# Kernel tuning notes

Hardware: AMD Instinct MI355X
Metric: run time of the kernel (lower is better)

The kernel has to match this reference:

```python
import jax, jax.numpy as jnp
import numpy as np

NUM_HEADS = 6
KERNEL = 5
EPS = 1e-6


def _neighbor_idx(L, k):
    # NATTEN neighborhood: window start clamped so every query has exactly k neighbors
    starts = jnp.clip(jnp.arange(L) - k // 2, 0, L - k)
    return starts[:, None] + jnp.arange(k)  # [L, k]


def ada_rmsnorm(x, scale, w1, b1, w2, b2):
    # x: [B,C,D,H,W]; RMS over spatial dims, gamma from channel means via small MLP
    rms = jnp.sqrt(jnp.mean(x * x, axis=(2, 3, 4), keepdims=True) + EPS)
    xn = x / rms
    stats = jnp.mean(x, axis=(2, 3, 4))                 # [B,C]
    h = jax.nn.relu(stats @ w1.T + b1)                  # [B,2C]
    gamma = jax.nn.sigmoid(h @ w2.T + b2)               # [B,C]
    return xn * (scale * gamma[:, :, None, None, None])


def reference(x, scale1, n1_w1, n1_b1, n1_w2, n1_b2,
              qkv_w, qkv_b, proj_w, proj_b,
              scale2, n2_w1, n2_b1, n2_w2, n2_b2,
              mlp_w1, mlp_b1, mlp_w2, mlp_b2):
    B, C, D, H, W = x.shape
    nh_, k_ = NUM_HEADS, KERNEL
    hd = C // nh_
    K3 = k_ ** 3

    # --- norm1 + neighborhood attention ---
    h = ada_rmsnorm(x, scale1, n1_w1, n1_b1, n1_w2, n1_b2)
    t = jnp.transpose(h, (0, 2, 3, 4, 1))               # [B,D,H,W,C]
    qkv = t @ qkv_w.T + qkv_b                           # [B,D,H,W,3C]
    q, k, v = jnp.split(qkv, 3, axis=-1)
    q = q.reshape(B, D, H, W, nh_, hd)
    k = k.reshape(B, D, H, W, nh_, hd)
    v = v.reshape(B, D, H, W, nh_, hd)

    iD = _neighbor_idx(D, k_)
    iH = _neighbor_idx(H, k_)
    iW = _neighbor_idx(W, k_)
    nd = iD[:, None, None, :, None, None]               # [D,1,1,k,1,1]
    nhh = iH[None, :, None, None, :, None]              # [1,H,1,1,k,1]
    nw = iW[None, None, :, None, None, :]               # [1,1,W,1,1,k]

    k_nb = k[:, nd, nhh, nw].reshape(B, D, H, W, K3, nh_, hd)
    v_nb = v[:, nd, nhh, nw].reshape(B, D, H, W, K3, nh_, hd)

    scale_qk = hd ** -0.5
    scores = jnp.einsum('bdhwnc,bdhwknc->bdhwnk', q, k_nb) * scale_qk  # [B,D,H,W,heads,K3]
    p = jax.nn.softmax(scores, axis=-1)
    o = jnp.einsum('bdhwnk,bdhwknc->bdhwnc', p, v_nb).reshape(B, D, H, W, C)
    o = o @ proj_w.T + proj_b                            # output projection
    x = x + jnp.transpose(o, (0, 4, 1, 2, 3))

    # --- norm2 + 1x1-conv MLP (GELU exact) ---
    h2 = ada_rmsnorm(x, scale2, n2_w1, n2_b1, n2_w2, n2_b2)
    m = jnp.einsum('oc,bcdhw->bodhw', mlp_w1, h2) + mlp_b1[None, :, None, None, None]
    m = jax.nn.gelu(m, approximate=False)
    m = jnp.einsum('oc,bcdhw->bodhw', mlp_w2, m) + mlp_b2[None, :, None, None, None]
    return x + m


def setup_inputs() -> dict:
    key = jax.random.key(0)
    ks = jax.random.split(key, 16)
    B, C, D, H, W = 1, 192, 16, 16, 16
    hid = 2 * C
    mlp_h = int(4.0 * C)
    s = 0.02
    inp = {
        'x': jax.random.normal(ks[0], (B, C, D, H, W), jnp.float32),
        'scale1': jnp.ones((1, C, 1, 1, 1), jnp.float32),
        'n1_w1': jax.random.normal(ks[1], (hid, C), jnp.float32) * s,
        'n1_b1': jnp.zeros((hid,), jnp.float32),
        'n1_w2': jax.random.normal(ks[2], (C, hid), jnp.float32) * s,
        'n1_b2': jnp.zeros((C,), jnp.float32),
        'qkv_w': jax.random.normal(ks[3], (3 * C, C), jnp.float32) * s,
        'qkv_b': jnp.zeros((3 * C,), jnp.float32),
        'proj_w': jax.random.normal(ks[4], (C, C), jnp.float32) * s,
        'proj_b': jnp.zeros((C,), jnp.float32),
        'scale2': jnp.ones((1, C, 1, 1, 1), jnp.float32),
        'n2_w1': jax.random.normal(ks[5], (hid, C), jnp.float32) * s,
        'n2_b1': jnp.zeros((hid,), jnp.float32),
        'n2_w2': jax.random.normal(ks[6], (C, hid), jnp.float32) * s,
        'n2_b2': jnp.zeros((C,), jnp.float32),
        'mlp_w1': jax.random.normal(ks[7], (mlp_h, C), jnp.float32) * s,
        'mlp_b1': jnp.zeros((mlp_h,), jnp.float32),
        'mlp_w2': jax.random.normal(ks[8], (C, mlp_h), jnp.float32) * s,
        'mlp_b2': jnp.zeros((C,), jnp.float32),
    }
    return inp
```

## Files before the change

### kernel.cpp

```cpp
#include <hip/hip_runtime.h>
#include <hip/hip_bf16.h>
#include <cmath>


#define NPOS 4096
#define C_CH 192
#define NB   512

typedef __bf16 bf16x8 __attribute__((ext_vector_type(8)));
typedef __bf16 bf16x4 __attribute__((ext_vector_type(4)));
typedef float  f32x4  __attribute__((ext_vector_type(4)));

__device__ __forceinline__ float bflo(unsigned int u) {
    union { unsigned int i; float f; } c; c.i = u << 16; return c.f;
}
__device__ __forceinline__ float bfhi(unsigned int u) {
    union { unsigned int i; float f; } c; c.i = u & 0xffff0000u; return c.f;
}


__device__ __forceinline__ void pre_sync(unsigned* bar, int grp) {
    __syncthreads();
    if (threadIdx.x == 0) {
        unsigned* arr    = bar + 128 + grp * 16;
        unsigned* master = bar + 256;
        unsigned* go     = bar + 272 + grp * 16;
        unsigned prev = __hip_atomic_fetch_add(arr, 1u, __ATOMIC_RELAXED,
                                               __HIP_MEMORY_SCOPE_AGENT);
        if (prev == 63u) {
            __hip_atomic_fetch_add(master, 1u, __ATOMIC_RELAXED,
                                   __HIP_MEMORY_SCOPE_AGENT);
            while (__hip_atomic_load(master, __ATOMIC_RELAXED,
                                     __HIP_MEMORY_SCOPE_AGENT) < 8u)
                __builtin_amdgcn_s_sleep(2);
            __hip_atomic_store(go, 1u, __ATOMIC_RELAXED, __HIP_MEMORY_SCOPE_AGENT);
        }
        while (__hip_atomic_load(go, __ATOMIC_RELAXED,
                                 __HIP_MEMORY_SCOPE_AGENT) == 0u)
            __builtin_amdgcn_s_sleep(2);
    }
    __syncthreads();
}

__device__ __forceinline__ void grid_sync(unsigned* bar, int idx, int xcc,
                                          unsigned myPop, unsigned nx) {
    __syncthreads();
    if (threadIdx.x == 0) {
        unsigned* base   = bar + 512 + idx * 512;
        unsigned* arr    = base + xcc * 16;
        unsigned* master = base + 128;
        unsigned* go     = base + 144 + xcc * 16;
        unsigned prev = __hip_atomic_fetch_add(arr, 1u, __ATOMIC_RELAXED,
                                               __HIP_MEMORY_SCOPE_AGENT);
        if (prev == myPop - 1u) {
            __hip_atomic_fetch_add(master, 1u, __ATOMIC_RELEASE,
                                   __HIP_MEMORY_SCOPE_AGENT);
            while (__hip_atomic_load(master, __ATOMIC_RELAXED,
                                     __HIP_MEMORY_SCOPE_AGENT) < nx)
                __builtin_amdgcn_s_sleep(2);
            __hip_atomic_store(go, 1u, __ATOMIC_RELAXED, __HIP_MEMORY_SCOPE_AGENT);
        }
        while (__hip_atomic_load(go, __ATOMIC_RELAXED,
                                 __HIP_MEMORY_SCOPE_AGENT) == 0u)
            __builtin_amdgcn_s_sleep(2);
    }
    __syncthreads();
}

__device__ __forceinline__ void conv_unit(const float* __restrict__ src,
                                          __bf16* __restrict__ dst, int base)
{
    int i = (base * 256 + (int)threadIdx.x) * 4;
    float4 v = *(const float4*)(src + i);
    bf16x4 o = { (__bf16)v.x, (__bf16)v.y, (__bf16)v.z, (__bf16)v.w };
    *(bf16x4*)(dst + i) = o;
}

__device__ void stats_unit(float* sm, const float* __restrict__ x,
                           float* __restrict__ sums, float* __restrict__ sumsq, int c)
{
    const float4* xc = (const float4*)(x + (size_t)c * NPOS);
    float a = 0.f, a2 = 0.f;
    for (int i = threadIdx.x; i < NPOS / 4; i += 256) {
        float4 v = xc[i];
        a  += v.x + v.y + v.z + v.w;
        a2 += v.x * v.x + v.y * v.y + v.z * v.z + v.w * v.w;
    }
    #pragma unroll
    for (int off = 32; off > 0; off >>= 1) {
        a  += __shfl_down(a, off);
        a2 += __shfl_down(a2, off);
    }
    float* ls = sm; float* ls2 = sm + 4;
    int wid = threadIdx.x >> 6;
    if ((threadIdx.x & 63) == 0) { ls[wid] = a; ls2[wid] = a2; }
    __syncthreads();
    if (threadIdx.x == 0) {
        float t = 0.f, t2 = 0.f;
        #pragma unroll
        for (int w = 0; w < 4; w++) { t += ls[w]; t2 += ls2[w]; }
        sums[c] = t; sumsq[c] = t2;
    }
    __syncthreads();
}

__device__ void convx_body(float* sm, const float* __restrict__ x,
    const float* __restrict__ sums, const float* __restrict__ sumsq,
    const float* __restrict__ scale,
    const __bf16* __restrict__ w1b, const float* __restrict__ b1,
    const __bf16* __restrict__ w2b, const float* __restrict__ b2,
    __bf16* __restrict__ xb, int p0)
{
    float* stats = sm;
    float* h     = sm + 192;
    float* gsl   = sm + 576;
    float* lds   = sm + 768;
    int t = threadIdx.x;

    if (t < C_CH)
        stats[t] = __hip_atomic_load((const float*)&sums[t], __ATOMIC_RELAXED,
                                     __HIP_MEMORY_SCOPE_AGENT) * (1.0f / (float)NPOS);
    __syncthreads();
    for (int j = t; j < 384; j += 256) {
        float acc = b1[j];
        const __bf16* wr = w1b + (size_t)j * C_CH;
        #pragma unroll 4
        for (int c = 0; c < C_CH; c += 8) {
            bf16x8 w8 = *(const bf16x8*)(wr + c);
            acc += (float)w8[0] * stats[c]     + (float)w8[1] * stats[c + 1]
                 + (float)w8[2] * stats[c + 2] + (float)w8[3] * stats[c + 3]
                 + (float)w8[4] * stats[c + 4] + (float)w8[5] * stats[c + 5]
                 + (float)w8[6] * stats[c + 6] + (float)w8[7] * stats[c + 7];
        }
        h[j] = fmaxf(acc, 0.0f);
    }
    __syncthreads();
    if (t < C_CH) {
        float acc = b2[t];
        const __bf16* wr = w2b + (size_t)t * 384;
        #pragma unroll 4
        for (int j = 0; j < 384; j += 8) {
            bf16x8 w8 = *(const bf16x8*)(wr + j);
            acc += (float)w8[0] * h[j]     + (float)w8[1] * h[j + 1]
                 + (float)w8[2] * h[j + 2] + (float)w8[3] * h[j + 3]
                 + (float)w8[4] * h[j + 4] + (float)w8[5] * h[j + 5]
                 + (float)w8[6] * h[j + 6] + (float)w8[7] * h[j + 7];
        }
        float g = 1.0f / (1.0f + __expf(-acc));
        float sq = __hip_atomic_load((const float*)&sumsq[t], __ATOMIC_RELAXED,
                                     __HIP_MEMORY_SCOPE_AGENT);
        float rms = sqrtf(sq * (1.0f / (float)NPOS) + 1e-6f);
        gsl[t] = scale[t] * g / rms;
    }
    __syncthreads();
    for (int idx = t; idx < 192 * 4; idx += 256) {
        int row = idx >> 2, p4 = idx & 3;
        float4 v = *(const float4*)(x + (size_t)row * NPOS + p0 + p4 * 4);
        float g = gsl[row];
        lds[row * 17 + p4 * 4 + 0] = v.x * g;
        lds[row * 17 + p4 * 4 + 1] = v.y * g;
        lds[row * 17 + p4 * 4 + 2] = v.z * g;
        lds[row * 17 + p4 * 4 + 3] = v.w * g;
    }
    __syncthreads();
    for (int idx = t; idx < 48 * 16; idx += 256) {
        int c4 = idx >> 4, p = idx & 15;
        bf16x4 o;
        #pragma unroll
        for (int j = 0; j < 4; j++) o[j] = (__bf16)lds[(c4 * 4 + j) * 17 + p];
        *(bf16x4*)(xb + (size_t)(p0 + p) * 192 + c4 * 4) = o;
    }
    __syncthreads();
}

template <int K, int EPI>
__device__ void gemm_tile(__bf16* al, __bf16* bl, int bx, int by,
    const __bf16* __restrict__ W, const float* __restrict__ bias,
    const __bf16* __restrict__ X, void* __restrict__ out,
    const float* __restrict__ resid, int M, __bf16* __restrict__ out_kv,
    float* __restrict__ s2sum, float* __restrict__ s2sq)
{
    constexpr int KC  = 192;
    constexpr int LDA = 200;
    int t    = threadIdx.x;
    int lane = t & 63;
    int wv   = t >> 6;
    int r16  = lane & 15;
    int quad = lane >> 4;
    int wvm  = wv >> 1;
    int wvn  = wv & 1;
    int mBase = by * 64;
    int nBase = bx * 64;

    f32x4 acc[2][2];
    #pragma unroll
    for (int i = 0; i < 2; i++)
        #pragma unroll
        for (int j = 0; j < 2; j++)
            acc[i][j] = (f32x4){0.f, 0.f, 0.f, 0.f};

    for (int k0 = 0; k0 < K; k0 += KC) {
        #pragma unroll
        for (int it = 0; it < 6; it++) {
            int c = it * 256 + t;
            int row = c / 24, off = c - row * 24;
            bf16x8 va = *(const bf16x8*)(W + (size_t)(mBase + row) * K + k0 + off * 8);
            *(bf16x8*)(al + row * LDA + off * 8) = va;
            bf16x8 vb = *(const bf16x8*)(X + (size_t)(nBase + row) * K + k0 + off * 8);
            *(bf16x8*)(bl + row * LDA + off * 8) = vb;
        }
        __syncthreads();
        #pragma unroll
        for (int ks = 0; ks < KC / 32; ks++) {
            bf16x8 a0 = *(const bf16x8*)(al + (wvm * 32 + r16) * LDA + ks * 32 + quad * 8);
            bf16x8 a1 = *(const bf16x8*)(al + (wvm * 32 + 16 + r16) * LDA + ks * 32 + quad * 8);
            bf16x8 b0 = *(const bf16x8*)(bl + (wvn * 32 + r16) * LDA + ks * 32 + quad * 8);
            bf16x8 b1 = *(const bf16x8*)(bl + (wvn * 32 + 16 + r16) * LDA + ks * 32 + quad * 8);
            acc[0][0] = __builtin_amdgcn_mfma_f32_16x16x32_bf16(a0, b0, acc[0][0], 0, 0, 0);
            acc[0][1] = __builtin_amdgcn_mfma_f32_16x16x32_bf16(a0, b1, acc[0][1], 0, 0, 0);
            acc[1][0] = __builtin_amdgcn_mfma_f32_16x16x32_bf16(a1, b0, acc[1][0], 0, 0, 0);
            acc[1][1] = __builtin_amdgcn_mfma_f32_16x16x32_bf16(a1, b1, acc[1][1], 0, 0, 0);
        }
        __syncthreads();
    }

    #pragma unroll
    for (int rt = 0; rt < 2; rt++) {
        int m0 = mBase + wvm * 32 + rt * 16 + quad * 4;
        float b0 = bias[m0], b1v = bias[m0 + 1], b2v = bias[m0 + 2], b3v = bias[m0 + 3];
        float ss[4] = {0.f, 0.f, 0.f, 0.f}, sq[4] = {0.f, 0.f, 0.f, 0.f};
        #pragma unroll
        for (int ct = 0; ct < 2; ct++) {
            int n = nBase + wvn * 32 + ct * 16 + r16;
            f32x4 a4 = acc[rt][ct];
            float g0 = a4[0] + b0, g1 = a4[1] + b1v, g2 = a4[2] + b2v, g3 = a4[3] + b3v;
            if (EPI == 0) {
                int sect = m0 / 192;
                int o0 = m0 - sect * 192;
                if (sect == 0) {
                    const float qs = 0.17677669529663687f;
                    *(float4*)((float*)out + (size_t)n * 192 + o0) =
                        make_float4(g0 * qs, g1 * qs, g2 * qs, g3 * qs);
                } else {
                    bf16x4 kvv = { (__bf16)g0, (__bf16)g1, (__bf16)g2, (__bf16)g3 };
                    *(bf16x4*)(out_kv + (size_t)n * 384 + (o0 >> 2) * 8 + (sect - 1) * 4) = kvv;
                }
            } else if (EPI == 2 || EPI == 4) {
                float* o = (float*)out;
                size_t i0 = (size_t)m0 * NPOS + n;
                float v0 = g0 + resid[i0];
                float v1 = g1 + resid[i0 + NPOS];
                float v2 = g2 + resid[i0 + 2 * NPOS];
                float v3 = g3 + resid[i0 + 3 * NPOS];
                o[i0] = v0; o[i0 + NPOS] = v1; o[i0 + 2 * NPOS] = v2; o[i0 + 3 * NPOS] = v3;
                if (EPI == 4) {
                    ss[0] += v0; sq[0] += v0 * v0;
                    ss[1] += v1; sq[1] += v1 * v1;
                    ss[2] += v2; sq[2] += v2 * v2;
                    ss[3] += v3; sq[3] += v3 * v3;
                }
            } else {
                bf16x4 v;
                v[0] = (__bf16)(0.5f * g0 * (1.0f + erff(g0 * 0.7071067811865475f)));
                v[1] = (__bf16)(0.5f * g1 * (1.0f + erff(g1 * 0.7071067811865475f)));
                v[2] = (__bf16)(0.5f * g2 * (1.0f + erff(g2 * 0.7071067811865475f)));
                v[3] = (__bf16)(0.5f * g3 * (1.0f + erff(g3 * 0.7071067811865475f)));
                *(bf16x4*)((__bf16*)out + (size_t)n * M + m0) = v;
            }
        }
        if (EPI == 4) {
            #pragma unroll
            for (int j = 0; j < 4; j++) {
                float s = ss[j], s2v = sq[j];
                #pragma unroll
                for (int off = 8; off >= 1; off >>= 1) {
                    s   += __shfl_down(s, off);
                    s2v += __shfl_down(s2v, off);
                }
                if (r16 == 0) {
                    atomicAdd(&s2sum[m0 + j], s);
                    atomicAdd(&s2sq[m0 + j], s2v);
                }
            }
        }
    }
}

__device__ __forceinline__ void attn_unit(const float* __restrict__ q,
    const __bf16* __restrict__ kv, __bf16* __restrict__ o, int unit)
{
    int t = threadIdx.x;
    int pairIdx = unit * 8 + (t >> 5);
    int sg   = (t >> 3) & 3;
    int lane = t & 7;
    int pos = pairIdx / 6;
    int head = pairIdx - pos * 6;
    int wq = pos & 15;
    int hq = (pos >> 4) & 15;
    int dq = pos >> 8;
    int d0 = min(max(dq - 2, 0), 11);
    int h0 = min(max(hq - 2, 0), 11);
    int w0 = min(max(wq - 2, 0), 11);

    const __bf16* kvb = kv + head * 64 + lane * 8;
    float4 q4 = *(const float4*)(q + (size_t)pos * 192 + head * 32 + lane * 4);

    float l = 0.0f;
    float4 acc = make_float4(0.f, 0.f, 0.f, 0.f);

    for (int dh = sg; dh < 25; dh += 4) {
        int di = dh / 5;
        int hi = dh - di * 5;
        int np0 = (d0 + di) * 256 + (h0 + hi) * 16 + w0;
        const __bf16* p = kvb + (size_t)np0 * 384;
        #pragma unroll
        for (int wi = 0; wi < 5; wi++) {
            uint4 u = *(const uint4*)p;
            float s = q4.x * bflo(u.x) + q4.y * bfhi(u.x)
                    + q4.z * bflo(u.y) + q4.w * bfhi(u.y);
            s += __shfl_xor(s, 1);
            s += __shfl_xor(s, 2);
            s += __shfl_xor(s, 4);
            float pr = __expf(s);
            l += pr;
            acc.x += pr * bflo(u.z);
            acc.y += pr * bfhi(u.z);
            acc.z += pr * bflo(u.w);
            acc.w += pr * bfhi(u.w);
            p += 384;
        }
    }

    #pragma unroll
    for (int off = 8; off <= 16; off <<= 1) {
        l     += __shfl_xor(l, off);
        acc.x += __shfl_xor(acc.x, off);
        acc.y += __shfl_xor(acc.y, off);
        acc.z += __shfl_xor(acc.z, off);
        acc.w += __shfl_xor(acc.w, off);
    }

    if (sg == 0) {
        float rl = 1.0f / l;
        bf16x4 ov = { (__bf16)(acc.x * rl), (__bf16)(acc.y * rl),
                      (__bf16)(acc.z * rl), (__bf16)(acc.w * rl) };
        *(bf16x4*)(o + (size_t)pos * 192 + head * 32 + lane * 4) = ov;
    }
}

__global__ __launch_bounds__(256) void fused(
    const float* __restrict__ x, const float* __restrict__ scale1,
    const float* __restrict__ n1_w1, const float* __restrict__ n1_b1,
    const float* __restrict__ n1_w2, const float* __restrict__ n1_b2,
    const float* __restrict__ qkv_w, const float* __restrict__ qkv_b,
    const float* __restrict__ proj_w, const float* __restrict__ proj_b,
    const float* __restrict__ scale2,
    const float* __restrict__ n2_w1, const float* __restrict__ n2_b1,
    const float* __restrict__ n2_w2, const float* __restrict__ n2_b2,
    const float* __restrict__ mlp_w1, const float* __restrict__ mlp_b1,
    const float* __restrict__ mlp_w2, const float* __restrict__ mlp_b2,
    float* __restrict__ ws, float* __restrict__ x2)
{
    __shared__ __align__(16) char smraw[51200];
    __bf16* al  = (__bf16*)smraw;
    __bf16* bl  = al + 64 * 200;
    float*  smf = (float*)smraw;

    float*  q_buf   = ws;
    __bf16* kv_buf  = (__bf16*)(ws + 786432);
    __bf16* xb      = (__bf16*)(ws + 2359296);
    __bf16* o_attn  = (__bf16*)(ws + 2752512);
    __bf16* qkv_wb  = (__bf16*)(ws + 3145728);
    __bf16* proj_wb = qkv_wb + 110592;
    __bf16* m1_wb   = proj_wb + 36864;
    __bf16* m2_wb   = m1_wb + 147456;
    float*  sums1   = ws + 3366912;
    float*  sumsq1  = ws + 3367104;
    float*  sums2   = ws + 3367296;
    float*  sumsq2  = ws + 3367488;
    __bf16* n1w1b   = (__bf16*)(ws + 3367680);
    __bf16* n1w2b   = n1w1b + 73728;
    __bf16* n2w1b   = n1w2b + 73728;
    __bf16* n2w2b   = n2w1b + 73728;
    unsigned* bar   = (unsigned*)(ws + 3515136);
    __bf16* m_buf   = (__bf16*)(ws + 3520512);
    __bf16* xb2     = (__bf16*)(ws + 5093376);

    int bid = blockIdx.x;
    int t   = threadIdx.x;

    int xcc = __builtin_amdgcn_s_getreg(63508) & 7;

    if (t == 0)
        __hip_atomic_fetch_add(bar + xcc * 16, 1u, __ATOMIC_RELAXED,
                               __HIP_MEMORY_SCOPE_AGENT);
    pre_sync(bar, bid & 7);
    unsigned myPop = 0, nx = 0;
    if (t == 0) {
        myPop = __hip_atomic_load(bar + xcc * 16, __ATOMIC_RELAXED,
                                  __HIP_MEMORY_SCOPE_AGENT);
        #pragma unroll
        for (int xi = 0; xi < 8; xi++)
            nx += (__hip_atomic_load(bar + xi * 16, __ATOMIC_RELAXED,
                                     __HIP_MEMORY_SCOPE_AGENT) > 0u) ? 1u : 0u;
    }

    for (int u = bid; u < 913; u += NB) {
        if      (u < 108) conv_unit(qkv_w,  qkv_wb, u);
        else if (u < 144) conv_unit(proj_w, proj_wb, u - 108);
        else if (u < 288) conv_unit(mlp_w1, m1_wb, u - 144);
        else if (u < 432) conv_unit(mlp_w2, m2_wb, u - 288);
        else if (u < 504) conv_unit(n1_w1,  n1w1b, u - 432);
        else if (u < 576) conv_unit(n1_w2,  n1w2b, u - 504);
        else if (u < 648) conv_unit(n2_w1,  n2w1b, u - 576);
        else if (u < 720) conv_unit(n2_w2,  n2w2b, u - 648);
        else if (u < 912) stats_unit(smf, x, sums1, sumsq1, u - 720);
        else {
            if (t < 192) {
                __hip_atomic_store(&sums2[t], 0.f, __ATOMIC_RELAXED,
                                   __HIP_MEMORY_SCOPE_AGENT);
                __hip_atomic_store(&sumsq2[t], 0.f, __ATOMIC_RELAXED,
                                   __HIP_MEMORY_SCOPE_AGENT);
            }
        }
    }
    grid_sync(bar, 0, xcc, myPop, nx);

    if (bid < 256)
        convx_body(smf, x, sums1, sumsq1, scale1, n1w1b, n1_b1, n1w2b, n1_b2, xb, bid * 16);
    grid_sync(bar, 1, xcc, myPop, nx);

    for (int tile = bid; tile < 576; tile += NB)
        gemm_tile<192, 0>(al, bl, tile & 63, tile >> 6, qkv_wb, qkv_b, xb,
                          (void*)q_buf, nullptr, 576, kv_buf, nullptr, nullptr);
    grid_sync(bar, 2, xcc, myPop, nx);

    {
        int base = (bid & 7) * 384 + (bid >> 3) * 6;
        for (int i = 0; i < 6; i++)
            attn_unit(q_buf, kv_buf, o_attn, base + i);
    }
    grid_sync(bar, 3, xcc, myPop, nx);

    if (bid < 192)
        gemm_tile<192, 4>(al, bl, bid & 63, bid >> 6, proj_wb, proj_b, o_attn,
                          (void*)x2, x, 192, nullptr, sums2, sumsq2);
    grid_sync(bar, 4, xcc, myPop, nx);

    if (bid < 256)
        convx_body(smf, x2, sums2, sumsq2, scale2, n2w1b, n2_b1, n2w2b, n2_b2, xb2, bid * 16);
    grid_sync(bar, 5, xcc, myPop, nx);

    for (int tile = bid; tile < 768; tile += NB)
        gemm_tile<192, 3>(al, bl, tile & 63, tile >> 6, m1_wb, mlp_b1, xb2,
                          (void*)m_buf, nullptr, 768, nullptr, nullptr, nullptr);
    grid_sync(bar, 6, xcc, myPop, nx);

    if (bid < 192)
        gemm_tile<768, 2>(al, bl, bid & 63, bid >> 6, m2_wb, mlp_b2, m_buf,
                          (void*)x2, x2, 192, nullptr, nullptr, nullptr);
}

extern "C" void kernel_launch(void* const* d_in, const int* in_sizes, int n_in,
                              void* d_out, int out_size, void* d_ws, size_t ws_size,
                              hipStream_t stream)
{
    const float* x      = (const float*)d_in[0];
    const float* scale1 = (const float*)d_in[1];
    const float* n1_w1  = (const float*)d_in[2];
    const float* n1_b1  = (const float*)d_in[3];
    const float* n1_w2  = (const float*)d_in[4];
    const float* n1_b2  = (const float*)d_in[5];
    const float* qkv_w  = (const float*)d_in[6];
    const float* qkv_b  = (const float*)d_in[7];
    const float* proj_w = (const float*)d_in[8];
    const float* proj_b = (const float*)d_in[9];
    const float* scale2 = (const float*)d_in[10];
    const float* n2_w1  = (const float*)d_in[11];
    const float* n2_b1  = (const float*)d_in[12];
    const float* n2_w2  = (const float*)d_in[13];
    const float* n2_b2  = (const float*)d_in[14];
    const float* mlp_w1 = (const float*)d_in[15];
    const float* mlp_b1 = (const float*)d_in[16];
    const float* mlp_w2 = (const float*)d_in[17];
    const float* mlp_b2 = (const float*)d_in[18];

    float* ws = (float*)d_ws;
    float* x2 = (float*)d_out;

    hipMemsetAsync(ws + 3515136, 0, 4096 * sizeof(unsigned), stream);

    fused<<<NB, 256, 0, stream>>>(x, scale1, n1_w1, n1_b1, n1_w2, n1_b2,
                                  qkv_w, qkv_b, proj_w, proj_b,
                                  scale2, n2_w1, n2_b1, n2_w2, n2_b2,
                                  mlp_w1, mlp_b1, mlp_w2, mlp_b2,
                                  ws, x2);
}
```

Measured before the change: 202.0 us.

## Fold adaptive RMSNorm scale into GEMM weights and drop two grid syncs

The per-channel RMSNorm gain is now applied to the weight tile as it is loaded into the qkv and MLP1 GEMMs. This lets the raw input transpose to bf16 run in the preprocessing phase, and the projection GEMM epilogue writes the bf16 transposed residual output directly. That removes the two standalone convx phases and two grid-wide barriers. In exchange every block recomputes the small gain MLP redundantly, and rounding changes slightly because scaling happens after bf16 conversion of x and on bf16 weights.

Measured after the change: 205.7 us. Within noise of the previous version (+1.8%).

```diff
diff --git a/kernel.cpp b/kernel.cpp
--- a/kernel.cpp
+++ b/kernel.cpp
@@ -104,19 +104,39 @@
     __syncthreads();
 }
 
-__device__ void convx_body(float* sm, const float* __restrict__ x,
+__device__ void transpose_unit(float* sm, const float* __restrict__ x,
+                               __bf16* __restrict__ xb, int p0)
+{
+    float* lds = sm;
+    int t = threadIdx.x;
+    for (int idx = t; idx < 192 * 4; idx += 256) {
+        int row = idx >> 2, p4 = idx & 3;
+        float4 v = *(const float4*)(x + (size_t)row * NPOS + p0 + p4 * 4);
+        lds[row * 17 + p4 * 4 + 0] = v.x;
+        lds[row * 17 + p4 * 4 + 1] = v.y;
+        lds[row * 17 + p4 * 4 + 2] = v.z;
+        lds[row * 17 + p4 * 4 + 3] = v.w;
+    }
+    __syncthreads();
+    for (int idx = t; idx < 48 * 16; idx += 256) {
+        int c4 = idx >> 4, p = idx & 15;
+        bf16x4 o;
+        #pragma unroll
+        for (int j = 0; j < 4; j++) o[j] = (__bf16)lds[(c4 * 4 + j) * 17 + p];
+        *(bf16x4*)(xb + (size_t)(p0 + p) * 192 + c4 * 4) = o;
+    }
+    __syncthreads();
+}
+
+__device__ void compute_gsl(float* scratch, float* gslOut,
     const float* __restrict__ sums, const float* __restrict__ sumsq,
     const float* __restrict__ scale,
     const __bf16* __restrict__ w1b, const float* __restrict__ b1,
-    const __bf16* __restrict__ w2b, const float* __restrict__ b2,
-    __bf16* __restrict__ xb, int p0)
-{
-    float* stats = sm;
-    float* h     = sm + 192;
-    float* gsl   = sm + 576;
-    float* lds   = sm + 768;
+    const __bf16* __restrict__ w2b, const float* __restrict__ b2)
+{
+    float* stats = scratch;
+    float* h     = scratch + 192;
     int t = threadIdx.x;
-
     if (t < C_CH)
         stats[t] = __hip_atomic_load((const float*)&sums[t], __ATOMIC_RELAXED,
                                      __HIP_MEMORY_SCOPE_AGENT) * (1.0f / (float)NPOS);
@@ -150,35 +170,19 @@
         float sq = __hip_atomic_load((const float*)&sumsq[t], __ATOMIC_RELAXED,
                                      __HIP_MEMORY_SCOPE_AGENT);
         float rms = sqrtf(sq * (1.0f / (float)NPOS) + 1e-6f);
-        gsl[t] = scale[t] * g / rms;
-    }
-    __syncthreads();
-    for (int idx = t; idx < 192 * 4; idx += 256) {
-        int row = idx >> 2, p4 = idx & 3;
-        float4 v = *(const float4*)(x + (size_t)row * NPOS + p0 + p4 * 4);
-        float g = gsl[row];
-        lds[row * 17 + p4 * 4 + 0] = v.x * g;
-        lds[row * 17 + p4 * 4 + 1] = v.y * g;
-        lds[row * 17 + p4 * 4 + 2] = v.z * g;
-        lds[row * 17 + p4 * 4 + 3] = v.w * g;
-    }
-    __syncthreads();
-    for (int idx = t; idx < 48 * 16; idx += 256) {
-        int c4 = idx >> 4, p = idx & 15;
-        bf16x4 o;
-        #pragma unroll
-        for (int j = 0; j < 4; j++) o[j] = (__bf16)lds[(c4 * 4 + j) * 17 + p];
-        *(bf16x4*)(xb + (size_t)(p0 + p) * 192 + c4 * 4) = o;
-    }
-    __syncthreads();
-}
-
-template <int K, int EPI>
-__device__ void gemm_tile(__bf16* al, __bf16* bl, int bx, int by,
+        gslOut[t] = scale[t] * g / rms;
+    }
+    __syncthreads();
+}
+
+template <int K, int EPI, bool SCALEA>
+__device__ void gemm_tile(__bf16* al, __bf16* bl, const float* gslLds,
+    int bx, int by,
     const __bf16* __restrict__ W, const float* __restrict__ bias,
     const __bf16* __restrict__ X, void* __restrict__ out,
     const float* __restrict__ resid, int M, __bf16* __restrict__ out_kv,
-    float* __restrict__ s2sum, float* __restrict__ s2sq)
+    float* __restrict__ s2sum, float* __restrict__ s2sq,
+    __bf16* __restrict__ xb2o)
 {
     constexpr int KC  = 192;
     constexpr int LDA = 200;
@@ -205,6 +209,11 @@
             int c = it * 256 + t;
             int row = c / 24, off = c - row * 24;
             bf16x8 va = *(const bf16x8*)(W + (size_t)(mBase + row) * K + k0 + off * 8);
+            if (SCALEA) {
+                #pragma unroll
+                for (int j = 0; j < 8; j++)
+                    va[j] = (__bf16)((float)va[j] * gslLds[off * 8 + j]);
+            }
             *(bf16x8*)(al + row * LDA + off * 8) = va;
             bf16x8 vb = *(const bf16x8*)(X + (size_t)(nBase + row) * K + k0 + off * 8);
             *(bf16x8*)(bl + row * LDA + off * 8) = vb;
@@ -254,6 +263,8 @@
                 float v3 = g3 + resid[i0 + 3 * NPOS];
                 o[i0] = v0; o[i0 + NPOS] = v1; o[i0 + 2 * NPOS] = v2; o[i0 + 3 * NPOS] = v3;
                 if (EPI == 4) {
+                    bf16x4 xv = { (__bf16)v0, (__bf16)v1, (__bf16)v2, (__bf16)v3 };
+                    *(bf16x4*)(xb2o + (size_t)n * 192 + m0) = xv;
                     ss[0] += v0; sq[0] += v0 * v0;
                     ss[1] += v1; sq[1] += v1 * v1;
                     ss[2] += v2; sq[2] += v2 * v2;
@@ -361,10 +372,11 @@
     const float* __restrict__ mlp_w2, const float* __restrict__ mlp_b2,
     float* __restrict__ ws, float* __restrict__ x2)
 {
-    __shared__ __align__(16) char smraw[51200];
-    __bf16* al  = (__bf16*)smraw;
-    __bf16* bl  = al + 64 * 200;
-    float*  smf = (float*)smraw;
+    __shared__ __align__(16) char smraw[52224];
+    __bf16* al     = (__bf16*)smraw;
+    __bf16* bl     = al + 64 * 200;
+    float*  smf    = (float*)smraw;
+    float*  gslLds = (float*)(smraw + 51200);
 
     float*  q_buf   = ws;
     __bf16* kv_buf  = (__bf16*)(ws + 786432);
@@ -405,17 +417,17 @@
                                      __HIP_MEMORY_SCOPE_AGENT) > 0u) ? 1u : 0u;
     }
 
-    for (int u = bid; u < 913; u += NB) {
-        if      (u < 108) conv_unit(qkv_w,  qkv_wb, u);
-        else if (u < 144) conv_unit(proj_w, proj_wb, u - 108);
-        else if (u < 288) conv_unit(mlp_w1, m1_wb, u - 144);
-        else if (u < 432) conv_unit(mlp_w2, m2_wb, u - 288);
-        else if (u < 504) conv_unit(n1_w1,  n1w1b, u - 432);
-        else if (u < 576) conv_unit(n1_w2,  n1w2b, u - 504);
-        else if (u < 648) conv_unit(n2_w1,  n2w1b, u - 576);
-        else if (u < 720) conv_unit(n2_w2,  n2w2b, u - 648);
-        else if (u < 912) stats_unit(smf, x, sums1, sumsq1, u - 720);
-        else {
+    for (int u = bid; u < 1169; u += NB) {
+        if      (u < 108)  conv_unit(qkv_w,  qkv_wb, u);
+        else if (u < 144)  conv_unit(proj_w, proj_wb, u - 108);
+        else if (u < 288)  conv_unit(mlp_w1, m1_wb, u - 144);
+        else if (u < 432)  conv_unit(mlp_w2, m2_wb, u - 288);
+        else if (u < 504)  conv_unit(n1_w1,  n1w1b, u - 432);
+        else if (u < 576)  conv_unit(n1_w2,  n1w2b, u - 504);
+        else if (u < 648)  conv_unit(n2_w1,  n2w1b, u - 576);
+        else if (u < 720)  conv_unit(n2_w2,  n2w2b, u - 648);
+        else if (u < 912)  stats_unit(smf, x, sums1, sumsq1, u - 720);
+        else if (u == 912) {
             if (t < 192) {
                 __hip_atomic_store(&sums2[t], 0.f, __ATOMIC_RELAXED,
                                    __HIP_MEMORY_SCOPE_AGENT);
@@ -423,42 +435,41 @@
                                    __HIP_MEMORY_SCOPE_AGENT);
             }
         }
+        else               transpose_unit(smf, x, xb, (u - 913) * 16);
     }
     grid_sync(bar, 0, xcc, myPop, nx);
 
-    if (bid < 256)
-        convx_body(smf, x, sums1, sumsq1, scale1, n1w1b, n1_b1, n1w2b, n1_b2, xb, bid * 16);
+    compute_gsl(smf, gslLds, sums1, sumsq1, scale1, n1w1b, n1_b1, n1w2b, n1_b2);
+    for (int tile = bid; tile < 576; tile += NB)
+        gemm_tile<192, 0, true>(al, bl, gslLds, tile & 63, tile >> 6,
+                                qkv_wb, qkv_b, xb, (void*)q_buf,
+                                nullptr, 576, kv_buf, nullptr, nullptr, nullptr);
     grid_sync(bar, 1, xcc, myPop, nx);
-
-    for (int tile = bid; tile < 576; tile += NB)
-        gemm_tile<192, 0>(al, bl, tile & 63, tile >> 6, qkv_wb, qkv_b, xb,
-                          (void*)q_buf, nullptr, 576, kv_buf, nullptr, nullptr);
-    grid_sync(bar, 2, xcc, myPop, nx);
 
     {
         int base = (bid & 7) * 384 + (bid >> 3) * 6;
         for (int i = 0; i < 6; i++)
             attn_unit(q_buf, kv_buf, o_attn, base + i);
     }
+    grid_sync(bar, 2, xcc, myPop, nx);
+
+    if (bid < 192)
+        gemm_tile<192, 4, false>(al, bl, nullptr, bid & 63, bid >> 6,
+                                 proj_wb, proj_b, o_attn, (void*)x2,
+                                 x, 192, nullptr, sums2, sumsq2, xb2);
     grid_sync(bar, 3, xcc, myPop, nx);
 
+    compute_gsl(smf, gslLds, sums2, sumsq2, scale2, n2w1b, n2_b1, n2w2b, n2_b2);
+    for (int tile = bid; tile < 768; tile += NB)
+        gemm_tile<192, 3, true>(al, bl, gslLds, tile & 63, tile >> 6,
+                                m1_wb, mlp_b1, xb2, (void*)m_buf,
+                                nullptr, 768, nullptr, nullptr, nullptr, nullptr);
+    grid_sync(bar, 4, xcc, myPop, nx);
+
     if (bid < 192)
-        gemm_tile<192, 4>(al, bl, bid & 63, bid >> 6, proj_wb, proj_b, o_attn,
-                          (void*)x2, x, 192, nullptr, sums2, sumsq2);
-    grid_sync(bar, 4, xcc, myPop, nx);
-
-    if (bid < 256)
-        convx_body(smf, x2, sums2, sumsq2, scale2, n2w1b, n2_b1, n2w2b, n2_b2, xb2, bid * 16);
-    grid_sync(bar, 5, xcc, myPop, nx);
-
-    for (int tile = bid; tile < 768; tile += NB)
-        gemm_tile<192, 3>(al, bl, tile & 63, tile >> 6, m1_wb, mlp_b1, xb2,
-                          (void*)m_buf, nullptr, 768, nullptr, nullptr, nullptr);
-    grid_sync(bar, 6, xcc, myPop, nx);
-
-    if (bid < 192)
-        gemm_tile<768, 2>(al, bl, bid & 63, bid >> 6, m2_wb, mlp_b2, m_buf,
-                          (void*)x2, x2, 192, nullptr, nullptr, nullptr);
+        gemm_tile<768, 2, false>(al, bl, nullptr, bid & 63, bid >> 6,
+                                 m2_wb, mlp_b2, m_buf, (void*)x2,
+                                 x2, 192, nullptr, nullptr, nullptr, nullptr);
 }
 
 extern "C" void kernel_launch(void* const* d_in, const int* in_sizes, int n_in,
@@ -488,7 +499,7 @@
     float* ws = (float*)d_ws;
     float* x2 = (float*)d_out;
 
-    hipMemsetAsync(ws + 3515136, 0, 4096 * sizeof(unsigned), stream);
+    hipMemsetAsync(ws + 3515136, 0, 3072 * sizeof(unsigned), stream);
 
     fused<<<NB, 256, 0, stream>>>(x, scale1, n1_w1, n1_b1, n1_w2, n1_b2,
                                   qkv_w, qkv_b, proj_w, proj_b,
```
